# Optimization experiments

Measured on AMD Instinct MI355X. Metric: run time of the kernel, lower is better.

The kernel has to match this reference:

```python
import jax, jax.numpy as jnp
import numpy as np

B, S, E, H, L = 4, 8192, 1024, 16, 64
D = E // H

def setup_inputs() -> dict:
    key = jax.random.key(0)
    ks = jax.random.split(key, 8)
    scale = 1.0 / np.sqrt(E)
    inp = {
        'query': jax.random.normal(ks[0], (B, S, E), jnp.float32),
        'key':   jax.random.normal(ks[1], (B, S, E), jnp.float32),
        'value': jax.random.normal(ks[2], (B, S, E), jnp.float32),
        'Wq': jax.random.normal(ks[3], (E, E), jnp.float32) * scale,
        'bq': jnp.zeros((E,), jnp.float32),
        'Wk': jax.random.normal(ks[4], (E, E), jnp.float32) * scale,
        'bk': jnp.zeros((E,), jnp.float32),
        'Wv': jax.random.normal(ks[5], (E, E), jnp.float32) * scale,
        'bv': jnp.zeros((E,), jnp.float32),
        'Wo': jax.random.normal(ks[6], (E, E), jnp.float32) * scale,
        'bo': jnp.zeros((E,), jnp.float32),
    }
    return inp

def reference(query, key, value, Wq, bq, Wk, bk, Wv, bv, Wo, bo):
    b, s, _ = query.shape
    # projections (torch Linear: x @ W.T + b), split heads -> [B, H, S, D]
    def split(x):
        return x.reshape(b, s, H, D).transpose(0, 2, 1, 3)
    q = split(query @ Wq.T + bq)
    k = split(key   @ Wk.T + bk)
    v = split(value @ Wv.T + bv)
    # landmark selection: key-norms averaged over heads -> [B, S], topk L per batch
    scores = jnp.linalg.norm(k, axis=-1).mean(axis=1)        # [B, S]
    _, idx = jax.lax.top_k(scores, L)                        # [B, L]
    # gather landmark K/V -> [B, H, L, D]
    gidx = idx[:, None, :, None]                             # [B, 1, L, 1]
    k_sp = jnp.take_along_axis(k, gidx, axis=2)
    v_sp = jnp.take_along_axis(v, gidx, axis=2)
    # attention over landmarks only
    attn = jnp.einsum('bhsd,bhld->bhsl', q, k_sp) / jnp.sqrt(jnp.asarray(D, q.dtype))
    w = jax.nn.softmax(attn, axis=-1)                        # [B, H, S, L]
    out = jnp.einsum('bhsl,bhld->bhsd', w, v_sp)             # [B, H, S, D]
    out = out.transpose(0, 2, 1, 3).reshape(b, s, E)
    out = out @ Wo.T + bo
    return (out, w)
```

## Files before the change

### kernel.cpp

```cpp
#include <hip/hip_runtime.h>
#include <cstdint>

typedef unsigned short u16;
typedef __attribute__((ext_vector_type(8))) short short8;
typedef __attribute__((ext_vector_type(4))) float f32x4;

#define AS1 __attribute__((address_space(1)))
#define AS3 __attribute__((address_space(3)))

#define BB 4
#define SS 8192
#define EE 1024
#define HH 16
#define DD 64
#define LL 64
#define CANDN 96

__device__ __forceinline__ void async16(const void* g, void* l) {
  __builtin_amdgcn_global_load_lds((const AS1 uint32_t*)g, (AS3 uint32_t*)l, 16, 0, 0);
}
__device__ __forceinline__ u16 f2b(float f) {
  uint32_t u = __float_as_uint(f);
  return (u16)((u + 0x7fffu + ((u >> 16) & 1u)) >> 16);
}
__device__ __forceinline__ float b2f(u16 h) { return __uint_as_float(((uint32_t)h) << 16); }

__global__ __launch_bounds__(256) void cvt_bf16_k(const float* __restrict__ in, u16* __restrict__ out, int n4) {
  int i = blockIdx.x * 256 + threadIdx.x;
  if (i >= n4) return;
  float4 v = ((const float4*)in)[i];
  ushort4 o;
  o.x = f2b(v.x); o.y = f2b(v.y); o.z = f2b(v.z); o.w = f2b(v.w);
  ((ushort4*)out)[i] = o;
}

__global__ __launch_bounds__(512) void gemm256(const u16* __restrict__ A, const u16* __restrict__ W,
                                               const float* __restrict__ bias,
                                               float* __restrict__ Cf, u16* __restrict__ Cb,
                                               float* __restrict__ scA, int K) {
  extern __shared__ __align__(16) u16 lds_[];
  u16* lA = lds_;
  u16* lB = lds_ + 3 * 16384;
  const int tid = threadIdx.x;
  const int wv = tid >> 6, lane = tid & 63;
  const int quad = lane >> 4, l15 = lane & 15;
  const int wm = wv >> 1, wn = wv & 1;

  const int nwg = gridDim.x * gridDim.y;
  int g = blockIdx.y * gridDim.x + blockIdx.x;
  int bx = blockIdx.x, by = blockIdx.y;
  if ((nwg & 7) == 0) {
    const int chunk = nwg >> 3;
    const int v = (g & 7) * chunk + (g >> 3);
    bx = v % gridDim.x;
    by = v / gridDim.x;
  }
  const int mt = by * 256, nt = bx * 128;

  const int rl = tid >> 3;
  const int g8 = (((tid & 7) ^ (rl & 7))) * 8;
  const u16* sA00 = A + (size_t)(mt + rl) * K + g8;
  const u16* sA01 = A + (size_t)(mt + 64 + rl) * K + g8;
  const u16* sA10 = A + (size_t)(mt + 128 + rl) * K + g8;
  const u16* sA11 = A + (size_t)(mt + 192 + rl) * K + g8;
  const u16* sB0  = W + (size_t)(nt + rl) * K + g8;
  const u16* sB1  = W + (size_t)(nt + 64 + rl) * K + g8;
  const int dA = tid * 8;
  const int dB = tid * 8;

  auto STAGE = [&](int tile, int pb) {
    const int off = tile * 64;
    async16(sA00 + off, lA + pb * 16384 + dA);
    async16(sA01 + off, lA + pb * 16384 + dA + 4096);
    async16(sA10 + off, lA + pb * 16384 + 8192 + dA);
    async16(sA11 + off, lA + pb * 16384 + 8192 + dA + 4096);
    async16(sB0 + off, lB + pb * 8192 + dB);
    async16(sB1 + off, lB + pb * 8192 + dB + 4096);
  };

  f32x4 acc[4][4];
#pragma unroll
  for (int i = 0; i < 4; i++)
#pragma unroll
    for (int j = 0; j < 4; j++) acc[i][j] = (f32x4){0.f, 0.f, 0.f, 0.f};

  const int NT = K >> 6;
  STAGE(0, 0);
  STAGE(1, 1);
  asm volatile("s_waitcnt vmcnt(6)\n\ts_barrier" ::: "memory");

  int pb = 0;
  for (int t = 0; t < NT; ++t) {
    if (t + 2 < NT) {
      int ps = pb + 2; if (ps >= 3) ps -= 3;
      STAGE(t + 2, ps);
    }
    const short8* pA = (const short8*)(lA + pb * 16384);
    const short8* pB = (const short8*)(lB + pb * 8192);
    short8 af[2][4], bf[2][4];
#pragma unroll
    for (int i = 0; i < 4; i++) {
      const int r = 64 * wm + 16 * i + l15;
      af[0][i] = pA[r * 8 + (quad ^ (r & 7))];
      af[1][i] = pA[r * 8 + ((quad + 4) ^ (r & 7))];
      const int rb = 64 * wn + 16 * i + l15;
      bf[0][i] = pB[rb * 8 + (quad ^ (rb & 7))];
      bf[1][i] = pB[rb * 8 + ((quad + 4) ^ (rb & 7))];
    }
    __builtin_amdgcn_s_setprio(1);
#pragma unroll
    for (int i = 0; i < 4; i++)
#pragma unroll
      for (int j = 0; j < 4; j++)
        acc[i][j] = __builtin_amdgcn_mfma_f32_16x16x32_bf16(af[0][i], bf[0][j], acc[i][j], 0, 0, 0);
#pragma unroll
    for (int i = 0; i < 4; i++)
#pragma unroll
      for (int j = 0; j < 4; j++)
        acc[i][j] = __builtin_amdgcn_mfma_f32_16x16x32_bf16(af[1][i], bf[1][j], acc[i][j], 0, 0, 0);
    __builtin_amdgcn_s_setprio(0);
    if (t + 1 < NT) {
      if (t + 2 < NT) { asm volatile("s_waitcnt vmcnt(6)\n\ts_barrier" ::: "memory"); }
      else            { asm volatile("s_waitcnt vmcnt(0)\n\ts_barrier" ::: "memory"); }
    }
    pb = pb + 1; if (pb == 3) pb = 0;
  }

  float bs[4];
#pragma unroll
  for (int j = 0; j < 4; j++) bs[j] = bias[nt + 64 * wn + 16 * j + l15];
#pragma unroll
  for (int i = 0; i < 4; i++) {
#pragma unroll
    for (int r = 0; r < 4; r++) {
      const int gm = mt + 64 * wm + 16 * i + quad * 4 + r;
      float nrm = 0.f;
#pragma unroll
      for (int j = 0; j < 4; j++) {
        float v = acc[i][j][r] + bs[j];
        const int gn = nt + 64 * wn + 16 * j + l15;
        if (Cf) Cf[(size_t)gm * EE + gn] = v;
        if (Cb) Cb[(size_t)gm * EE + gn] = f2b(v);
        nrm += v * v;
      }
      if (scA) {
#pragma unroll
        for (int m = 1; m < 16; m <<= 1) nrm += __shfl_xor(nrm, m, 64);
        if (l15 == 0) atomicAdd(&scA[gm], sqrtf(nrm) * (1.f / 16.f));
      }
    }
  }
}

#define TKT 1024
#define EQCAP 256
__global__ __launch_bounds__(TKT) void topk1_k(const float* __restrict__ sc, int* __restrict__ cand) {
  const int b = blockIdx.x;
  __shared__ uint32_t s[SS];
  __shared__ int wsum[TKT / 64];
  __shared__ int cnt_sh;
  __shared__ int counter, eqcount;
  __shared__ int eqbuf[EQCAP];
  const int tid = threadIdx.x;
  const int lane = tid & 63, wv = tid >> 6;
  for (int i = tid; i < SS; i += TKT) s[i] = __float_as_uint(sc[b * SS + i]);
  if (tid == 0) { counter = 0; eqcount = 0; }
  __syncthreads();

  uint32_t lo = 0u, hi = 0x7f7fffffu;
  while (lo < hi) {
    uint32_t mid = lo + ((hi - lo + 1) >> 1);
    int c = 0;
    for (int i = tid; i < SS; i += TKT) c += (s[i] >= mid) ? 1 : 0;
#pragma unroll
    for (int m = 1; m < 64; m <<= 1) c += __shfl_xor(c, m, 64);
    if (lane == 0) wsum[wv] = c;
    __syncthreads();
    if (tid == 0) {
      int t = 0;
#pragma unroll
      for (int w = 0; w < TKT / 64; w++) t += wsum[w];
      cnt_sh = t;
    }
    __syncthreads();
    if (cnt_sh >= CANDN) lo = mid; else hi = mid - 1;
    __syncthreads();
  }
  const uint32_t T = lo;

  for (int i = tid; i < SS; i += TKT) {
    uint32_t u = s[i];
    if (u > T) {
      int p = atomicAdd(&counter, 1);
      cand[b * CANDN + p] = i;
    } else if (u == T) {
      int p = atomicAdd(&eqcount, 1);
      if (p < EQCAP) eqbuf[p] = i;
    }
  }
  __syncthreads();
  const int above = counter;
  const int rem = CANDN - above;
  int ec = eqcount; if (ec > EQCAP) ec = EQCAP;
  __syncthreads();
  for (int i = tid; i < ec; i += TKT) {
    int me = eqbuf[i];
    int rank = 0;
    for (int j = 0; j < ec; j++) rank += (eqbuf[j] < me) ? 1 : 0;
    if (rank < rem) {
      int p = atomicAdd(&counter, 1);
      cand[b * CANDN + p] = me;
    }
  }
}

__global__ __launch_bounds__(256) void rescore_k(const float* __restrict__ key, const float* __restrict__ Wk,
                                                 const int* __restrict__ cand, double* __restrict__ kpart) {
  const int kc = blockIdx.x, h = blockIdx.y, b = blockIdx.z;
  const int d = threadIdx.x & 63, cg = threadIdx.x >> 6;
  __shared__ float wk[64 * 257];
  __shared__ float xs[24 * 256];
  for (int i = threadIdx.x; i < 64 * 256; i += 256)
    wk[(i >> 8) * 257 + (i & 255)] = Wk[(size_t)(h * 64 + (i >> 8)) * EE + kc * 256 + (i & 255)];
  for (int c0 = 0; c0 < CANDN; c0 += 24) {
    __syncthreads();
    for (int i = threadIdx.x; i < 24 * 256; i += 256) {
      int c = c0 + (i >> 8);
      xs[i] = key[((size_t)b * SS + cand[b * CANDN + c]) * EE + kc * 256 + (i & 255)];
    }
    __syncthreads();
    double acc[6] = {0, 0, 0, 0, 0, 0};
    for (int kk = 0; kk < 256; kk++) {
      double wv_ = (double)wk[d * 257 + kk];
#pragma unroll
      for (int j = 0; j < 6; j++)
        acc[j] += wv_ * (double)xs[(cg * 6 + j) * 256 + kk];
    }
#pragma unroll
    for (int j = 0; j < 6; j++) {
      int c = c0 + cg * 6 + j;
      kpart[(((size_t)kc * BB + b) * CANDN + c) * 1024 + h * 64 + d] = acc[j];
    }
  }
}

__global__ __launch_bounds__(64) void score2_k(const double* __restrict__ kpart, const float* __restrict__ bk,
                                               double* __restrict__ sc2) {
  const int c = blockIdx.x, b = blockIdx.y;
  const int lane = threadIdx.x;
  double tot = 0.0;
  for (int h = 0; h < HH; h++) {
    double v = (double)bk[h * 64 + lane];
#pragma unroll
    for (int kc = 0; kc < 4; kc++)
      v += kpart[(((size_t)kc * BB + b) * CANDN + c) * 1024 + h * 64 + lane];
    double s = v * v;
#pragma unroll
    for (int m = 1; m < 64; m <<= 1) s += __shfl_xor(s, m, 64);
    tot += sqrt(s);
  }
  if (lane == 0) sc2[b * CANDN + c] = tot * (1.0 / 16.0);
}

__global__ __launch_bounds__(128) void topk2_k(const double* __restrict__ sc2, const int* __restrict__ cand,
                                               int* __restrict__ idxf) {
  const int b = blockIdx.x, t = threadIdx.x;
  if (t >= CANDN) return;
  double my = sc2[b * CANDN + t];
  int mi = cand[b * CANDN + t];
  int rank = 0;
  for (int j = 0; j < CANDN; j++) {
    double sj = sc2[b * CANDN + j];
    int ij = cand[b * CANDN + j];
    if (sj > my || (sj == my && ij < mi)) rank++;
  }
  if (rank < LL) idxf[b * LL + rank] = mi;
}

__global__ __launch_bounds__(256) void gatherx_k(const float* __restrict__ value, const int* __restrict__ idxf,
                                                 u16* __restrict__ xg) {
  const int r = blockIdx.x;
  const int b = r >> 6;
  const float* src = value + ((size_t)b * SS + idxf[r]) * EE;
  for (int i = threadIdx.x; i < EE; i += 256) xg[(size_t)r * EE + i] = f2b(src[i]);
}

__global__ __launch_bounds__(64) void gathersp_k(const u16* __restrict__ kb, const float* __restrict__ vg,
                                                 const int* __restrict__ idxf,
                                                 u16* __restrict__ ksp, u16* __restrict__ vspT) {
  const int g = blockIdx.x;
  const int l = g & 63, h = (g >> 6) & 15, b = g >> 10;
  const int d = threadIdx.x;
  ksp[(size_t)g * 64 + d] = kb[((size_t)b * SS + idxf[b * 64 + l]) * EE + h * 64 + d];
  vspT[((size_t)(b * 16 + h) * 64 + d) * 64 + l] = f2b(vg[((size_t)b * 64 + l) * EE + h * 64 + d]);
}

__global__ __launch_bounds__(256) void attn_k(const u16* __restrict__ qb, const u16* __restrict__ ksp,
                                              const u16* __restrict__ vspT,
                                              float* __restrict__ wout, u16* __restrict__ attnb) {
  __shared__ __align__(16) u16 qt[4096];
  __shared__ __align__(16) u16 kt[4096];
  __shared__ __align__(16) u16 vt[4096];
  __shared__ __align__(16) u16 wt[4096];
  const int tid = threadIdx.x;
  const int wv = tid >> 6, lane = tid & 63, quad = lane >> 4, l15 = lane & 15;
  const int s0 = blockIdx.x * 64;
  const int bh = blockIdx.y, b = bh >> 4, h = bh & 15;

  {
    const int bi0 = tid, bi1 = 256 + tid;
    const int r0 = bi0 >> 3, c0 = (bi0 & 7) ^ (r0 & 7);
    const int r1 = bi1 >> 3, c1 = (bi1 & 7) ^ (r1 & 7);
    const u16* qg = qb + ((size_t)b * SS + s0) * EE + h * 64;
    async16(qg + (size_t)r0 * EE + c0 * 8, qt + bi0 * 8);
    async16(qg + (size_t)r1 * EE + c1 * 8, qt + bi1 * 8);
    const u16* kg = ksp + (size_t)bh * 4096;
    async16(kg + r0 * 64 + c0 * 8, kt + bi0 * 8);
    async16(kg + r1 * 64 + c1 * 8, kt + bi1 * 8);
    const u16* vgp = vspT + (size_t)bh * 4096;
    async16(vgp + r0 * 64 + c0 * 8, vt + bi0 * 8);
    async16(vgp + r1 * 64 + c1 * 8, vt + bi1 * 8);
  }
  __syncthreads();

  f32x4 acc[4];
#pragma unroll
  for (int j = 0; j < 4; j++) acc[j] = (f32x4){0.f, 0.f, 0.f, 0.f};
  const int ar = 16 * wv + l15;
#pragma unroll
  for (int ks = 0; ks < 2; ks++) {
    const int cg = quad + ks * 4;
    short8 af = ((const short8*)qt)[ar * 8 + (cg ^ (ar & 7))];
#pragma unroll
    for (int j = 0; j < 4; j++) {
      int br = 16 * j + l15;
      short8 bf = ((const short8*)kt)[br * 8 + (cg ^ (br & 7))];
      acc[j] = __builtin_amdgcn_mfma_f32_16x16x32_bf16(af, bf, acc[j], 0, 0, 0);
    }
  }
#pragma unroll
  for (int j = 0; j < 4; j++) acc[j] *= 0.125f;

  float inv[4];
#pragma unroll
  for (int r = 0; r < 4; r++) {
    float m = fmaxf(fmaxf(acc[0][r], acc[1][r]), fmaxf(acc[2][r], acc[3][r]));
#pragma unroll
    for (int msk = 1; msk < 16; msk <<= 1) m = fmaxf(m, __shfl_xor(m, msk, 64));
    float e0 = __expf(acc[0][r] - m);
    float e1 = __expf(acc[1][r] - m);
    float e2 = __expf(acc[2][r] - m);
    float e3 = __expf(acc[3][r] - m);
    acc[0][r] = e0; acc[1][r] = e1; acc[2][r] = e2; acc[3][r] = e3;
    float s = e0 + e1 + e2 + e3;
#pragma unroll
    for (int msk = 1; msk < 16; msk <<= 1) s += __shfl_xor(s, msk, 64);
    inv[r] = 1.f / s;
  }

  const size_t wbase = ((size_t)bh * SS + s0 + 16 * wv) * 64;
#pragma unroll
  for (int j = 0; j < 4; j++) {
#pragma unroll
    for (int r = 0; r < 4; r++) {
      float val = acc[j][r] * inv[r];
      int rowl = quad * 4 + r;
      int l = 16 * j + l15;
      wout[wbase + (size_t)rowl * 64 + l] = val;
      int wr = 16 * wv + rowl;
      wt[wr * 64 + ((l >> 3) ^ (wr & 7)) * 8 + (l & 7)] = f2b(val);
    }
  }
  __syncthreads();

  f32x4 acc2[4];
#pragma unroll
  for (int j = 0; j < 4; j++) acc2[j] = (f32x4){0.f, 0.f, 0.f, 0.f};
#pragma unroll
  for (int ks = 0; ks < 2; ks++) {
    const int cg = quad + ks * 4;
    short8 af = ((const short8*)wt)[ar * 8 + (cg ^ (ar & 7))];
#pragma unroll
    for (int j = 0; j < 4; j++) {
      int br = 16 * j + l15;
      short8 bf = ((const short8*)vt)[br * 8 + (cg ^ (br & 7))];
      acc2[j] = __builtin_amdgcn_mfma_f32_16x16x32_bf16(af, bf, acc2[j], 0, 0, 0);
    }
  }
#pragma unroll
  for (int j = 0; j < 4; j++)
#pragma unroll
    for (int r = 0; r < 4; r++)
      attnb[((size_t)b * SS + s0 + 16 * wv + quad * 4 + r) * EE + h * 64 + 16 * j + l15] = f2b(acc2[j][r]);
}

extern "C" void kernel_launch(void* const* d_in, const int* in_sizes, int n_in,
                              void* d_out, int out_size, void* d_ws, size_t ws_size,
                              hipStream_t stream) {
  (void)in_sizes; (void)n_in; (void)out_size; (void)ws_size;
  const float* query = (const float*)d_in[0];
  const float* key   = (const float*)d_in[1];
  const float* value = (const float*)d_in[2];
  const float* Wq = (const float*)d_in[3];
  const float* bq = (const float*)d_in[4];
  const float* Wk = (const float*)d_in[5];
  const float* bk = (const float*)d_in[6];
  const float* Wv = (const float*)d_in[7];
  const float* bv = (const float*)d_in[8];
  const float* Wo = (const float*)d_in[9];
  const float* bo = (const float*)d_in[10];
  float* out = (float*)d_out;
  float* wout = out + (size_t)BB * SS * EE;

  char* p = (char*)d_ws;
  auto alloc = [&](size_t n) { char* r = p; p += (n + 255) & ~(size_t)255; return r; };
  u16* qbf = (u16*)alloc((size_t)BB * SS * EE * 2);
  u16* kbf = (u16*)alloc((size_t)BB * SS * EE * 2);
  u16* wqb = (u16*)alloc((size_t)EE * EE * 2);
  u16* wkb = (u16*)alloc((size_t)EE * EE * 2);
  u16* wvb = (u16*)alloc((size_t)EE * EE * 2);
  u16* wob = (u16*)alloc((size_t)EE * EE * 2);
  u16* qb  = (u16*)alloc((size_t)BB * SS * EE * 2);
  u16* kb  = (u16*)alloc((size_t)BB * SS * EE * 2);
  float*  sc    = (float*)alloc((size_t)BB * SS * 4);
  int*    cand  = (int*)alloc(BB * CANDN * 4);
  double* kpart = (double*)alloc((size_t)4 * BB * CANDN * 1024 * 8);
  double* sc2   = (double*)alloc(BB * CANDN * 8);
  int*    idxf  = (int*)alloc(BB * LL * 4);
  u16*    xg    = (u16*)alloc((size_t)BB * LL * EE * 2);
  float*  vg    = (float*)alloc((size_t)BB * LL * EE * 4);
  u16*    ksp   = (u16*)alloc((size_t)BB * HH * LL * DD * 2);
  u16*    vspT  = (u16*)alloc((size_t)BB * HH * DD * LL * 2);
  u16*    attnb = qbf;

  const int M = BB * SS;
  const size_t gemm_lds = 147456;

  cvt_bf16_k<<<(M * EE / 4 + 255) / 256, 256, 0, stream>>>(query, qbf, M * EE / 4);
  cvt_bf16_k<<<(M * EE / 4 + 255) / 256, 256, 0, stream>>>(key, kbf, M * EE / 4);
  cvt_bf16_k<<<(EE * EE / 4 + 255) / 256, 256, 0, stream>>>(Wq, wqb, EE * EE / 4);
  cvt_bf16_k<<<(EE * EE / 4 + 255) / 256, 256, 0, stream>>>(Wk, wkb, EE * EE / 4);
  cvt_bf16_k<<<(EE * EE / 4 + 255) / 256, 256, 0, stream>>>(Wv, wvb, EE * EE / 4);
  cvt_bf16_k<<<(EE * EE / 4 + 255) / 256, 256, 0, stream>>>(Wo, wob, EE * EE / 4);
  hipMemsetAsync(sc, 0, (size_t)M * 4, stream);

  dim3 gg(EE / 128, M / 256);
  gemm256<<<gg, 512, gemm_lds, stream>>>(qbf, wqb, bq, nullptr, qb, nullptr, EE);
  gemm256<<<gg, 512, gemm_lds, stream>>>(kbf, wkb, bk, nullptr, kb, sc, EE);

  topk1_k<<<BB, TKT, 0, stream>>>(sc, cand);
  rescore_k<<<dim3(4, HH, BB), 256, 0, stream>>>(key, Wk, cand, kpart);
  score2_k<<<dim3(CANDN, BB), 64, 0, stream>>>(kpart, bk, sc2);
  topk2_k<<<BB, 128, 0, stream>>>(sc2, cand, idxf);

  gatherx_k<<<BB * LL, 256, 0, stream>>>(value, idxf, xg);
  gemm256<<<dim3(EE / 128, BB * LL / 256), 512, gemm_lds, stream>>>(xg, wvb, bv, vg, nullptr, nullptr, EE);
  gathersp_k<<<BB * HH * LL, 64, 0, stream>>>(kb, vg, idxf, ksp, vspT);

  attn_k<<<dim3(SS / 64, BB * HH), 256, 0, stream>>>(qb, ksp, vspT, wout, attnb);

  gemm256<<<gg, 512, gemm_lds, stream>>>(attnb, wob, bo, out, nullptr, nullptr, EE);
}
```

Baseline: 969.9 us.

## Replace 256x128 GEMM with 128x128 tile, 4-stage pipeline, fused Q/K launch

The 256x128, 512-thread GEMM with a 3-stage 64-deep K pipeline becomes a 128x128, 256-thread kernel with a 4-stage 32-deep K pipeline and a new swizzle. The Q and K projections now run in one launch that selects operands by block row. The smaller LDS footprint (64KB) should let more workgroups run per CU, and merging the two launches fills the grid better. In exchange each tile reuses data less and the per-k-step barrier overhead is higher.

```diff
diff --git a/kernel.cpp b/kernel.cpp
--- a/kernel.cpp
+++ b/kernel.cpp
@@ -34,13 +34,13 @@
   ((ushort4*)out)[i] = o;
 }
 
-__global__ __launch_bounds__(512) void gemm256(const u16* __restrict__ A, const u16* __restrict__ W,
-                                               const float* __restrict__ bias,
-                                               float* __restrict__ Cf, u16* __restrict__ Cb,
-                                               float* __restrict__ scA, int K) {
+__global__ __launch_bounds__(256) void gemm128(
+    const u16* __restrict__ A0, const u16* __restrict__ W0, const float* __restrict__ b0,
+    float* __restrict__ Cf0, u16* __restrict__ Cb0, float* __restrict__ sc0,
+    const u16* __restrict__ A1, const u16* __restrict__ W1, const float* __restrict__ b1,
+    float* __restrict__ Cf1, u16* __restrict__ Cb1, float* __restrict__ sc1,
+    int mt0, int K) {
   extern __shared__ __align__(16) u16 lds_[];
-  u16* lA = lds_;
-  u16* lB = lds_ + 3 * 16384;
   const int tid = threadIdx.x;
   const int wv = tid >> 6, lane = tid & 63;
   const int quad = lane >> 4, l15 = lane & 15;
@@ -55,27 +55,26 @@
     bx = v % gridDim.x;
     by = v / gridDim.x;
   }
-  const int mt = by * 256, nt = bx * 128;
-
-  const int rl = tid >> 3;
-  const int g8 = (((tid & 7) ^ (rl & 7))) * 8;
-  const u16* sA00 = A + (size_t)(mt + rl) * K + g8;
-  const u16* sA01 = A + (size_t)(mt + 64 + rl) * K + g8;
-  const u16* sA10 = A + (size_t)(mt + 128 + rl) * K + g8;
-  const u16* sA11 = A + (size_t)(mt + 192 + rl) * K + g8;
-  const u16* sB0  = W + (size_t)(nt + rl) * K + g8;
-  const u16* sB1  = W + (size_t)(nt + 64 + rl) * K + g8;
-  const int dA = tid * 8;
-  const int dB = tid * 8;
+  const u16* A; const u16* W; const float* bias; float* Cf; u16* Cb; float* scA;
+  int myb;
+  if (by < mt0) { A = A0; W = W0; bias = b0; Cf = Cf0; Cb = Cb0; scA = sc0; myb = by; }
+  else          { A = A1; W = W1; bias = b1; Cf = Cf1; Cb = Cb1; scA = sc1; myb = by - mt0; }
+  const int mt = myb * 128, nt = bx * 128;
+
+  const int row0 = tid >> 2, cg0 = (tid & 3) ^ ((row0 >> 1) & 3);
+  const int row1 = 64 + row0, cg1 = (tid & 3) ^ ((row1 >> 1) & 3);
+  const u16* gA0 = A + (size_t)(mt + row0) * K + cg0 * 8;
+  const u16* gA1 = A + (size_t)(mt + row1) * K + cg1 * 8;
+  const u16* gB0 = W + (size_t)(nt + row0) * K + cg0 * 8;
+  const u16* gB1 = W + (size_t)(nt + row1) * K + cg1 * 8;
 
   auto STAGE = [&](int tile, int pb) {
-    const int off = tile * 64;
-    async16(sA00 + off, lA + pb * 16384 + dA);
-    async16(sA01 + off, lA + pb * 16384 + dA + 4096);
-    async16(sA10 + off, lA + pb * 16384 + 8192 + dA);
-    async16(sA11 + off, lA + pb * 16384 + 8192 + dA + 4096);
-    async16(sB0 + off, lB + pb * 8192 + dB);
-    async16(sB1 + off, lB + pb * 8192 + dB + 4096);
+    const int off = tile * 32;
+    u16* base = lds_ + pb * 8192;
+    async16(gA0 + off, base + tid * 8);
+    async16(gA1 + off, base + 2048 + tid * 8);
+    async16(gB0 + off, base + 4096 + tid * 8);
+    async16(gB1 + off, base + 6144 + tid * 8);
   };
 
   f32x4 acc[4][4];
@@ -84,46 +83,36 @@
 #pragma unroll
     for (int j = 0; j < 4; j++) acc[i][j] = (f32x4){0.f, 0.f, 0.f, 0.f};
 
-  const int NT = K >> 6;
+  const int NT = K >> 5;
   STAGE(0, 0);
   STAGE(1, 1);
-  asm volatile("s_waitcnt vmcnt(6)\n\ts_barrier" ::: "memory");
-
-  int pb = 0;
+  STAGE(2, 2);
+  asm volatile("s_waitcnt vmcnt(8)\n\ts_barrier" ::: "memory");
+
   for (int t = 0; t < NT; ++t) {
-    if (t + 2 < NT) {
-      int ps = pb + 2; if (ps >= 3) ps -= 3;
-      STAGE(t + 2, ps);
-    }
-    const short8* pA = (const short8*)(lA + pb * 16384);
-    const short8* pB = (const short8*)(lB + pb * 8192);
-    short8 af[2][4], bf[2][4];
+    if (t + 3 < NT) STAGE(t + 3, (t + 3) & 3);
+    const short8* pA = (const short8*)(lds_ + (t & 3) * 8192);
+    const short8* pB = pA + 512;
+    short8 af[4], bfr[4];
 #pragma unroll
     for (int i = 0; i < 4; i++) {
       const int r = 64 * wm + 16 * i + l15;
-      af[0][i] = pA[r * 8 + (quad ^ (r & 7))];
-      af[1][i] = pA[r * 8 + ((quad + 4) ^ (r & 7))];
+      af[i] = pA[r * 4 + (quad ^ ((r >> 1) & 3))];
       const int rb = 64 * wn + 16 * i + l15;
-      bf[0][i] = pB[rb * 8 + (quad ^ (rb & 7))];
-      bf[1][i] = pB[rb * 8 + ((quad + 4) ^ (rb & 7))];
+      bfr[i] = pB[rb * 4 + (quad ^ ((rb >> 1) & 3))];
     }
     __builtin_amdgcn_s_setprio(1);
 #pragma unroll
     for (int i = 0; i < 4; i++)
 #pragma unroll
       for (int j = 0; j < 4; j++)
-        acc[i][j] = __builtin_amdgcn_mfma_f32_16x16x32_bf16(af[0][i], bf[0][j], acc[i][j], 0, 0, 0);
-#pragma unroll
-    for (int i = 0; i < 4; i++)
-#pragma unroll
-      for (int j = 0; j < 4; j++)
-        acc[i][j] = __builtin_amdgcn_mfma_f32_16x16x32_bf16(af[1][i], bf[1][j], acc[i][j], 0, 0, 0);
+        acc[i][j] = __builtin_amdgcn_mfma_f32_16x16x32_bf16(af[i], bfr[j], acc[i][j], 0, 0, 0);
     __builtin_amdgcn_s_setprio(0);
     if (t + 1 < NT) {
-      if (t + 2 < NT) { asm volatile("s_waitcnt vmcnt(6)\n\ts_barrier" ::: "memory"); }
-      else            { asm volatile("s_waitcnt vmcnt(0)\n\ts_barrier" ::: "memory"); }
-    }
-    pb = pb + 1; if (pb == 3) pb = 0;
+      if (t + 3 < NT)      { asm volatile("s_waitcnt vmcnt(8)\n\ts_barrier" ::: "memory"); }
+      else if (t + 2 < NT) { asm volatile("s_waitcnt vmcnt(4)\n\ts_barrier" ::: "memory"); }
+      else                 { asm volatile("s_waitcnt vmcnt(0)\n\ts_barrier" ::: "memory"); }
+    }
   }
 
   float bs[4];
@@ -434,7 +423,7 @@
   u16*    attnb = qbf;
 
   const int M = BB * SS;
-  const size_t gemm_lds = 147456;
+  const size_t g128_lds = 65536;
 
   cvt_bf16_k<<<(M * EE / 4 + 255) / 256, 256, 0, stream>>>(query, qbf, M * EE / 4);
   cvt_bf16_k<<<(M * EE / 4 + 255) / 256, 256, 0, stream>>>(key, kbf, M * EE / 4);
@@ -444,9 +433,9 @@
   cvt_bf16_k<<<(EE * EE / 4 + 255) / 256, 256, 0, stream>>>(Wo, wob, EE * EE / 4);
   hipMemsetAsync(sc, 0, (size_t)M * 4, stream);
 
-  dim3 gg(EE / 128, M / 256);
-  gemm256<<<gg, 512, gemm_lds, stream>>>(qbf, wqb, bq, nullptr, qb, nullptr, EE);
-  gemm256<<<gg, 512, gemm_lds, stream>>>(kbf, wkb, bk, nullptr, kb, sc, EE);
+  gemm128<<<dim3(EE / 128, 2 * M / 128), 256, g128_lds, stream>>>(
+      qbf, wqb, bq, nullptr, qb, nullptr,
+      kbf, wkb, bk, nullptr, kb, sc, M / 128, EE);
 
   topk1_k<<<BB, TKT, 0, stream>>>(sc, cand);
   rescore_k<<<dim3(4, HH, BB), 256, 0, stream>>>(key, Wk, cand, kpart);
@@ -454,10 +443,14 @@
   topk2_k<<<BB, 128, 0, stream>>>(sc2, cand, idxf);
 
   gatherx_k<<<BB * LL, 256, 0, stream>>>(value, idxf, xg);
-  gemm256<<<dim3(EE / 128, BB * LL / 256), 512, gemm_lds, stream>>>(xg, wvb, bv, vg, nullptr, nullptr, EE);
+  gemm128<<<dim3(EE / 128, BB * LL / 128), 256, g128_lds, stream>>>(
+      xg, wvb, bv, vg, nullptr, nullptr,
+      xg, wvb, bv, vg, nullptr, nullptr, BB * LL / 128, EE);
   gathersp_k<<<BB * HH * LL, 64, 0, stream>>>(kb, vg, idxf, ksp, vspT);
 
   attn_k<<<dim3(SS / 64, BB * HH), 256, 0, stream>>>(qb, ksp, vspT, wout, attnb);
 
-  gemm256<<<gg, 512, gemm_lds, stream>>>(attnb, wob, bo, out, nullptr, nullptr, EE);
-}
+  gemm128<<<dim3(EE / 128, M / 128), 256, g128_lds, stream>>>(
+      attnb, wob, bo, out, nullptr, nullptr,
+      attnb, wob, bo, out, nullptr, nullptr, M / 128, EE);
+}
```

Measured after the change: 1.013 ms. 4.5% more time.
